# Performance work log

Measured on AMD Instinct MI355X. Metric: run time of the kernel, lower is better.

The kernel has to match this reference:

```python
import jax, jax.numpy as jnp
import numpy as np

B, NL, NT = 8, 64, 512   # graphs, ligand atoms/graph, target nodes/graph
CF = 128                 # per-node embedding dim (Linear(256,...) => 2*128)
H = 128                  # hidden_dim
K = 10                   # n_gaussians
E = 1024                 # ligand edges
BN_EPS = 1e-4


def setup_inputs() -> dict:
    key = jax.random.key(0)
    ks = jax.random.split(key, 24)
    inp = {}
    inp["h_l_x"] = jax.random.normal(ks[0], (B * NL, CF), jnp.float32)
    inp["h_t_x"] = jax.random.normal(ks[1], (B * NT, CF), jnp.float32)
    inp["h_l_pos"] = jax.random.normal(ks[2], (B * NL, 3), jnp.float32)
    inp["h_t_pos"] = jax.random.normal(ks[3], (B * NT, 3), jnp.float32)
    inp["edge_index"] = jax.random.randint(ks[4], (2, E), 0, B * NL, jnp.int64)
    s = 0.05
    inp["W1"] = jax.random.normal(ks[5], (2 * CF, H), jnp.float32) * s
    inp["b1"] = jnp.zeros((H,), jnp.float32)
    inp["gamma"] = jnp.ones((H,), jnp.float32)
    inp["beta"] = jnp.zeros((H,), jnp.float32)
    inp["rmean"] = jax.random.normal(ks[6], (H,), jnp.float32) * 0.1
    inp["rvar"] = jax.random.uniform(ks[7], (H,), jnp.float32, 0.5, 1.5)
    inp["Wpi"] = jax.random.normal(ks[8], (H, K), jnp.float32) * s
    inp["bpi"] = jnp.zeros((K,), jnp.float32)
    inp["Wsig"] = jax.random.normal(ks[9], (H, K), jnp.float32) * s
    inp["bsig"] = jnp.zeros((K,), jnp.float32)
    inp["Wmu"] = jax.random.normal(ks[10], (H, K), jnp.float32) * s
    inp["bmu"] = jnp.zeros((K,), jnp.float32)
    inp["Wat"] = jax.random.normal(ks[11], (CF, 28), jnp.float32) * s
    inp["bat"] = jnp.zeros((28,), jnp.float32)
    inp["Wbd"] = jax.random.normal(ks[12], (2 * CF, 6), jnp.float32) * s
    inp["bbd"] = jnp.zeros((6,), jnp.float32)
    return inp


def reference(h_l_x, h_t_x, h_l_pos, h_t_pos, edge_index,
              W1, b1, gamma, beta, rmean, rvar,
              Wpi, bpi, Wsig, bsig, Wmu, bmu, Wat, bat, Wbd, bbd):
    # dense batched node features (equal counts per graph => reshape)
    hl = h_l_x.reshape(B, NL, CF)
    ht = h_t_x.reshape(B, NT, CF)

    # cat([hl_repeat, ht_repeat]) @ W1 == hl@W1[:CF] + ht@W1[CF:] (broadcast add)
    zl = jnp.einsum('blc,ch->blh', hl, W1[:CF])          # [B,NL,H]
    zt = jnp.einsum('btc,ch->bth', ht, W1[CF:])          # [B,NT,H]
    z = zl[:, :, None, :] + zt[:, None, :, :] + b1       # [B,NL,NT,H]
    z = z.reshape(B * NL * NT, H)

    # BatchNorm1d (eval: running stats), ELU; Dropout is identity in eval
    z = (z - rmean) * (gamma / jnp.sqrt(rvar + BN_EPS)) + beta
    C = jax.nn.elu(z)

    pi = jax.nn.softmax(C @ Wpi + bpi, axis=-1)
    sigma = jax.nn.elu(C @ Wsig + bsig) + 1.1
    mu = jax.nn.elu(C @ Wmu + bmu) + 1.0

    # pairwise euclidean distances, detached in original
    pl = h_l_pos.reshape(B, NL, 3)
    pt = h_t_pos.reshape(B, NT, 3)
    d2 = (-2.0 * jnp.einsum('bld,btd->blt', pl, pt)
          + jnp.sum(pt ** 2, -1)[:, None, :]
          + jnp.sum(pl ** 2, -1)[:, :, None])
    dist = jnp.sqrt(d2).reshape(B * NL * NT)
    dist = jax.lax.stop_gradient(dist)[:, None]          # [P,1]

    atom_types = h_l_x @ Wat + bat                       # [B*NL,28]
    eb = jnp.concatenate([h_l_x[edge_index[0]], h_l_x[edge_index[1]]], axis=1)
    bond_types = eb @ Wbd + bbd                          # [E,6]

    C_batch = jnp.repeat(jnp.arange(B, dtype=jnp.int32), NL * NT)
    return (pi, sigma, mu, dist, atom_types, bond_types, C_batch)
```

## Files before the change

### kernel.cpp

```cpp
#include <hip/hip_runtime.h>
#include <cstdint>
#include <cstddef>

#define NB_B 8
#define NL   64
#define NT   512
#define CF   128
#define HD   128
#define NK   10
#define NE   1024

static constexpr size_t P_TOT    = (size_t)NB_B * NL * NT;
static constexpr size_t PI_OFF   = 0;
static constexpr size_t SIG_OFF  = P_TOT * 10;
static constexpr size_t MU_OFF   = SIG_OFF + P_TOT * 10;
static constexpr size_t DIST_OFF = MU_OFF + P_TOT * 10;
static constexpr size_t AT_OFF   = DIST_OFF + P_TOT;
static constexpr size_t BD_OFF   = AT_OFF + 512 * 28;
static constexpr size_t CB_OFF   = BD_OFF + NE * 6;

typedef __attribute__((ext_vector_type(8))) short short8;
typedef __attribute__((ext_vector_type(4))) float floatx4;
typedef __attribute__((ext_vector_type(2))) float floatx2;

__device__ __forceinline__ float bf2f(unsigned short u) {
    return __uint_as_float(((unsigned int)u) << 16);
}
__device__ __forceinline__ unsigned short f2bf(float f) {
    unsigned int x = __float_as_uint(f);
    x = (x + 0x7FFFu + ((x >> 16) & 1u)) >> 16;
    return (unsigned short)x;
}

__global__ __launch_bounds__(256) void k_pre(
    const float* __restrict__ hl,
    const float* __restrict__ ht,
    const int*   __restrict__ eidx,
    const float* __restrict__ W1,
    const float* __restrict__ b1,
    const float* __restrict__ gamma_,
    const float* __restrict__ beta_,
    const float* __restrict__ rmean,
    const float* __restrict__ rvar,
    const float* __restrict__ Wpi,
    const float* __restrict__ Wsig,
    const float* __restrict__ Wmu,
    const float* __restrict__ Wat,
    const float* __restrict__ bat,
    const float* __restrict__ Wbd,
    const float* __restrict__ bbd,
    unsigned short* __restrict__ zl,
    unsigned short* __restrict__ zt,
    unsigned short* __restrict__ wcomb,
    float* __restrict__ out_at,
    float* __restrict__ out_bd)
{
    const int blk = blockIdx.x;
    const int tid = threadIdx.x;

    if (blk < 576) {
        __shared__ float xs[8 * CF];
        const int r0 = blk * 8;
        const bool is_l = (r0 < 512);
        const float* src = is_l ? (hl + (size_t)r0 * CF)
                                : (ht + (size_t)(r0 - 512) * CF);
        for (int i = tid; i < 8 * CF; i += 256) xs[i] = src[i];
        __syncthreads();

        const int h  = tid & 127;
        const int rr = (tid >> 7) * 4;
        float a0 = 0.f, a1 = 0.f, a2 = 0.f, a3 = 0.f;
        const float* wp = W1 + (size_t)(is_l ? 0 : CF) * HD + h;
        #pragma unroll 4
        for (int c = 0; c < CF; ++c) {
            float w = wp[(size_t)c * HD];
            a0 += xs[(rr + 0) * CF + c] * w;
            a1 += xs[(rr + 1) * CF + c] * w;
            a2 += xs[(rr + 2) * CF + c] * w;
            a3 += xs[(rr + 3) * CF + c] * w;
        }
        const float s = gamma_[h] * rsqrtf(rvar[h] + 1e-4f);
        if (is_l) {
            zl[(size_t)(r0 + rr + 0) * HD + h] = f2bf(a0 * s);
            zl[(size_t)(r0 + rr + 1) * HD + h] = f2bf(a1 * s);
            zl[(size_t)(r0 + rr + 2) * HD + h] = f2bf(a2 * s);
            zl[(size_t)(r0 + rr + 3) * HD + h] = f2bf(a3 * s);
        } else {
            const float off = (b1[h] - rmean[h]) * s + beta_[h];
            const int rt = r0 - 512 + rr;
            zt[(size_t)(rt + 0) * HD + h] = f2bf(a0 * s + off);
            zt[(size_t)(rt + 1) * HD + h] = f2bf(a1 * s + off);
            zt[(size_t)(rt + 2) * HD + h] = f2bf(a2 * s + off);
            zt[(size_t)(rt + 3) * HD + h] = f2bf(a3 * s + off);
        }
    } else if (blk == 576) {
        for (int i = tid; i < HD * 32; i += 256) {
            int hh = i >> 5, n = i & 31;
            float v = 0.f;
            if (n < 10)      v = Wpi [hh * NK + n];
            else if (n < 20) v = Wsig[hh * NK + (n - 10)];
            else if (n < 30) v = Wmu [hh * NK + (n - 20)];
            wcomb[i] = f2bf(v);
        }
    } else if (blk < 633) {
        const int oi = (blk - 577) * 256 + tid;
        const int r = oi / 28, n = oi - r * 28;
        float acc = bat[n];
        #pragma unroll 4
        for (int c = 0; c < CF; ++c)
            acc += hl[(size_t)r * CF + c] * Wat[c * 28 + n];
        out_at[oi] = acc;
    } else {
        const int oi = (blk - 633) * 256 + tid;
        const int e = oi / 6, n = oi - e * 6;
        const int s0 = eidx[e], s1 = eidx[NE + e];
        float acc = bbd[n];
        #pragma unroll 4
        for (int c = 0; c < CF; ++c) {
            acc += hl[(size_t)s0 * CF + c] * Wbd[c * 6 + n];
            acc += hl[(size_t)s1 * CF + c] * Wbd[(CF + c) * 6 + n];
        }
        out_bd[oi] = acc;
    }
}

__global__ __launch_bounds__(256) void k_main(
    const unsigned short* __restrict__ zl,
    const unsigned short* __restrict__ zt,
    const unsigned short* __restrict__ wcomb,
    const float* __restrict__ bpi,
    const float* __restrict__ bsig,
    const float* __restrict__ bmu,
    const float* __restrict__ hlpos,
    const float* __restrict__ htpos,
    float* __restrict__ out)
{
    __shared__ unsigned short Cl[128 * 136];
    __shared__ float Dl[128 * 33];
    __shared__ float zls[HD];
    __shared__ float biass[32];
    __shared__ float pls[4];

    const int tid  = threadIdx.x;
    const int blk  = blockIdx.x;
    const int b    = blk >> 6;
    const int l    = blk & 63;
    const int lane = tid & 63;
    const int wave = tid >> 6;

    if (tid < 128) {
        zls[tid] = bf2f(zl[(size_t)(b * NL + l) * HD + tid]);
    } else if (tid < 160) {
        int n = tid - 128;
        float v = 0.f;
        if (n < 10)      v = bpi[n];
        else if (n < 20) v = bsig[n - 10];
        else if (n < 30) v = bmu[n - 20];
        biass[n] = v;
    } else if (tid < 163) {
        pls[tid - 160] = hlpos[(size_t)(b * NL + l) * 3 + (tid - 160)];
    }

    short8 bfrag[2][4];
    #pragma unroll
    for (int nt = 0; nt < 2; ++nt) {
        #pragma unroll
        for (int kb = 0; kb < 4; ++kb) {
            const int n = nt * 16 + (lane & 15);
            const int kbase = kb * 32 + (lane >> 4) * 8;
            #pragma unroll
            for (int j = 0; j < 8; ++j)
                bfrag[nt][kb][j] = (short)wcomb[(kbase + j) * 32 + n];
        }
    }
    __syncthreads();

    for (int ch = 0; ch < 4; ++ch) {
        const int tc = ch * 128;

        {
            const int p  = tid >> 1;
            const int h0 = (tid & 1) * 64;
            const unsigned short* ztr = zt + (size_t)(b * NT + tc + p) * HD + h0;
            #pragma unroll
            for (int hh = 0; hh < 64; hh += 8) {
                short8 zv = *(const short8*)(ztr + hh);
                short8 cv;
                #pragma unroll
                for (int e2 = 0; e2 < 8; ++e2) {
                    float a = zls[h0 + hh + e2] + bf2f((unsigned short)zv[e2]);
                    float c = (a > 0.f) ? a : (__expf(a) - 1.f);
                    cv[e2] = (short)f2bf(c);
                }
                *(short8*)(&Cl[p * 136 + h0 + hh]) = cv;
            }
        }
        __syncthreads();

        floatx4 acc[2][2];
        #pragma unroll
        for (int i = 0; i < 2; ++i)
            #pragma unroll
            for (int j = 0; j < 2; ++j)
                acc[i][j] = (floatx4){0.f, 0.f, 0.f, 0.f};

        const int m = lane & 15;
        #pragma unroll
        for (int kb = 0; kb < 4; ++kb) {
            const int ko = kb * 32 + (lane >> 4) * 8;
            short8 a0 = *(const short8*)(&Cl[(wave * 32 + m) * 136 + ko]);
            short8 a1 = *(const short8*)(&Cl[(wave * 32 + 16 + m) * 136 + ko]);
            #pragma unroll
            for (int nt = 0; nt < 2; ++nt) {
                acc[0][nt] = __builtin_amdgcn_mfma_f32_16x16x32_bf16(a0, bfrag[nt][kb], acc[0][nt], 0, 0, 0);
                acc[1][nt] = __builtin_amdgcn_mfma_f32_16x16x32_bf16(a1, bfrag[nt][kb], acc[1][nt], 0, 0, 0);
            }
        }
        #pragma unroll
        for (int pt = 0; pt < 2; ++pt)
            #pragma unroll
            for (int nt = 0; nt < 2; ++nt)
                #pragma unroll
                for (int r = 0; r < 4; ++r) {
                    const int row = wave * 32 + pt * 16 + (lane >> 4) * 4 + r;
                    const int col = nt * 16 + (lane & 15);
                    Dl[row * 33 + col] = acc[pt][nt][r];
                }
        __syncthreads();

        const size_t gp = ((size_t)(b * NL + l)) * NT + tc + (tid & 127);
        if (tid < 128) {
            const int p = tid;
            float v[10];
            float mx = -1e30f;
            #pragma unroll
            for (int n = 0; n < 10; ++n) {
                v[n] = Dl[p * 33 + n] + biass[n];
                mx = fmaxf(mx, v[n]);
            }
            float s = 0.f;
            #pragma unroll
            for (int n = 0; n < 10; ++n) { v[n] = __expf(v[n] - mx); s += v[n]; }
            const float inv = 1.f / s;
            floatx2* po = (floatx2*)(out + PI_OFF + gp * 10);
            #pragma unroll
            for (int n = 0; n < 5; ++n) po[n] = (floatx2){v[2*n] * inv, v[2*n+1] * inv};
        } else {
            const int p = tid - 128;
            float sg[10], mv[10];
            #pragma unroll
            for (int n = 0; n < 10; ++n) {
                float x = Dl[p * 33 + 10 + n] + biass[10 + n];
                sg[n] = ((x > 0.f) ? x : (__expf(x) - 1.f)) + 1.1f;
                float y = Dl[p * 33 + 20 + n] + biass[20 + n];
                mv[n] = ((y > 0.f) ? y : (__expf(y) - 1.f)) + 1.0f;
            }
            floatx2* ps = (floatx2*)(out + SIG_OFF + gp * 10);
            floatx2* pm = (floatx2*)(out + MU_OFF  + gp * 10);
            #pragma unroll
            for (int n = 0; n < 5; ++n) {
                ps[n] = (floatx2){sg[2*n], sg[2*n+1]};
                pm[n] = (floatx2){mv[2*n], mv[2*n+1]};
            }
            const int t = tc + p;
            const size_t pb = (size_t)(b * NT + t) * 3;
            const float dx = pls[0] - htpos[pb + 0];
            const float dy = pls[1] - htpos[pb + 1];
            const float dz = pls[2] - htpos[pb + 2];
            out[DIST_OFF + gp] = sqrtf(dx * dx + dy * dy + dz * dz);
            out[CB_OFF + gp]   = (float)b;
        }
        __syncthreads();
    }
}

extern "C" void kernel_launch(void* const* d_in, const int* in_sizes, int n_in,
                              void* d_out, int out_size, void* d_ws, size_t ws_size,
                              hipStream_t stream)
{
    const float* hl     = (const float*)d_in[0];
    const float* ht     = (const float*)d_in[1];
    const float* hlpos  = (const float*)d_in[2];
    const float* htpos  = (const float*)d_in[3];
    const int*   eidx   = (const int*)d_in[4];
    const float* W1     = (const float*)d_in[5];
    const float* b1     = (const float*)d_in[6];
    const float* gamma_ = (const float*)d_in[7];
    const float* beta_  = (const float*)d_in[8];
    const float* rmean  = (const float*)d_in[9];
    const float* rvar   = (const float*)d_in[10];
    const float* Wpi    = (const float*)d_in[11];
    const float* bpi    = (const float*)d_in[12];
    const float* Wsig   = (const float*)d_in[13];
    const float* bsig   = (const float*)d_in[14];
    const float* Wmu    = (const float*)d_in[15];
    const float* bmu    = (const float*)d_in[16];
    const float* Wat    = (const float*)d_in[17];
    const float* bat    = (const float*)d_in[18];
    const float* Wbd    = (const float*)d_in[19];
    const float* bbd    = (const float*)d_in[20];

    float* out = (float*)d_out;
    unsigned short* ws  = (unsigned short*)d_ws;
    unsigned short* zl    = ws;
    unsigned short* zt    = ws + 512 * 128;
    unsigned short* wcomb = ws + 512 * 128 + 4096 * 128;

    k_pre<<<657, 256, 0, stream>>>(hl, ht, eidx, W1, b1, gamma_, beta_, rmean, rvar,
                                   Wpi, Wsig, Wmu, Wat, bat, Wbd, bbd,
                                   zl, zt, wcomb, out + AT_OFF, out + BD_OFF);
    k_main<<<512, 256, 0, stream>>>(zl, zt, wcomb, bpi, bsig, bmu, hlpos, htpos, out);
}
```

Measured before the change: 139.6 us.

## Split main kernel per target chunk, build MFMA A-fragments in registers, MFMA pre-GEMM

k_main now launches one block per (graph, ligand atom, 128-target chunk) instead of looping over four chunks, so there are four times as many blocks and fewer serial iterations each. The ELU-activated C tile is built directly in registers from global zt and zl loads, skipping the LDS staging buffer and one barrier per chunk. The combined head weights are stored transposed so each B fragment is a single vector load. The zl/zt projection in k_pre moves from a scalar FP32 loop to bf16 MFMA with in-register conversion. The costs are redundant zl and bias loads across blocks and bf16 rounding of the inputs and W1 in the projection.

```diff
diff --git a/kernel.cpp b/kernel.cpp
--- a/kernel.cpp
+++ b/kernel.cpp
@@ -51,59 +51,87 @@
     const float* __restrict__ bbd,
     unsigned short* __restrict__ zl,
     unsigned short* __restrict__ zt,
-    unsigned short* __restrict__ wcomb,
+    unsigned short* __restrict__ wcomb_t,
     float* __restrict__ out_at,
     float* __restrict__ out_bd)
 {
     const int blk = blockIdx.x;
     const int tid = threadIdx.x;
 
-    if (blk < 576) {
-        __shared__ float xs[8 * CF];
-        const int r0 = blk * 8;
-        const bool is_l = (r0 < 512);
-        const float* src = is_l ? (hl + (size_t)r0 * CF)
-                                : (ht + (size_t)(r0 - 512) * CF);
-        for (int i = tid; i < 8 * CF; i += 256) xs[i] = src[i];
-        __syncthreads();
-
-        const int h  = tid & 127;
-        const int rr = (tid >> 7) * 4;
-        float a0 = 0.f, a1 = 0.f, a2 = 0.f, a3 = 0.f;
-        const float* wp = W1 + (size_t)(is_l ? 0 : CF) * HD + h;
-        #pragma unroll 4
-        for (int c = 0; c < CF; ++c) {
-            float w = wp[(size_t)c * HD];
-            a0 += xs[(rr + 0) * CF + c] * w;
-            a1 += xs[(rr + 1) * CF + c] * w;
-            a2 += xs[(rr + 2) * CF + c] * w;
-            a3 += xs[(rr + 3) * CF + c] * w;
-        }
-        const float s = gamma_[h] * rsqrtf(rvar[h] + 1e-4f);
-        if (is_l) {
-            zl[(size_t)(r0 + rr + 0) * HD + h] = f2bf(a0 * s);
-            zl[(size_t)(r0 + rr + 1) * HD + h] = f2bf(a1 * s);
-            zl[(size_t)(r0 + rr + 2) * HD + h] = f2bf(a2 * s);
-            zl[(size_t)(r0 + rr + 3) * HD + h] = f2bf(a3 * s);
-        } else {
-            const float off = (b1[h] - rmean[h]) * s + beta_[h];
-            const int rt = r0 - 512 + rr;
-            zt[(size_t)(rt + 0) * HD + h] = f2bf(a0 * s + off);
-            zt[(size_t)(rt + 1) * HD + h] = f2bf(a1 * s + off);
-            zt[(size_t)(rt + 2) * HD + h] = f2bf(a2 * s + off);
-            zt[(size_t)(rt + 3) * HD + h] = f2bf(a3 * s + off);
-        }
-    } else if (blk == 576) {
-        for (int i = tid; i < HD * 32; i += 256) {
-            int hh = i >> 5, n = i & 31;
+    if (blk < 144) {
+        const bool is_l = (blk < 16);
+        const int rbase = is_l ? blk * 32 : (blk - 16) * 32;
+        const float* A  = is_l ? hl : ht;
+        const float* Wx = W1 + (is_l ? 0 : (size_t)CF * HD);
+        unsigned short* Z = is_l ? zl : zt;
+
+        const int wave = tid >> 6;
+        const int lane = tid & 63;
+        const int m    = lane & 15;
+        const int kq   = (lane >> 4) * 8;
+        const int n0   = wave * 32 + m;
+
+        floatx4 acc[2][2];
+        #pragma unroll
+        for (int i = 0; i < 2; ++i)
+            #pragma unroll
+            for (int j = 0; j < 2; ++j)
+                acc[i][j] = (floatx4){0.f, 0.f, 0.f, 0.f};
+
+        #pragma unroll
+        for (int kb = 0; kb < 4; ++kb) {
+            const int k0 = kb * 32 + kq;
+            short8 a[2];
+            #pragma unroll
+            for (int mt = 0; mt < 2; ++mt) {
+                const float* ap = A + (size_t)(rbase + mt * 16 + m) * CF + k0;
+                floatx4 f0 = *(const floatx4*)ap;
+                floatx4 f1 = *(const floatx4*)(ap + 4);
+                #pragma unroll
+                for (int j = 0; j < 4; ++j) {
+                    a[mt][j]     = (short)f2bf(f0[j]);
+                    a[mt][4 + j] = (short)f2bf(f1[j]);
+                }
+            }
+            short8 bf[2];
+            #pragma unroll
+            for (int nt = 0; nt < 2; ++nt) {
+                const int n = n0 + nt * 16;
+                #pragma unroll
+                for (int j = 0; j < 8; ++j)
+                    bf[nt][j] = (short)f2bf(Wx[(size_t)(k0 + j) * HD + n]);
+            }
+            #pragma unroll
+            for (int mt = 0; mt < 2; ++mt)
+                #pragma unroll
+                for (int nt = 0; nt < 2; ++nt)
+                    acc[mt][nt] = __builtin_amdgcn_mfma_f32_16x16x32_bf16(a[mt], bf[nt], acc[mt][nt], 0, 0, 0);
+        }
+
+        #pragma unroll
+        for (int nt = 0; nt < 2; ++nt) {
+            const int col = n0 + nt * 16;
+            const float s   = gamma_[col] * rsqrtf(rvar[col] + 1e-4f);
+            const float off = is_l ? 0.f : ((b1[col] - rmean[col]) * s + beta_[col]);
+            #pragma unroll
+            for (int mt = 0; mt < 2; ++mt)
+                #pragma unroll
+                for (int r = 0; r < 4; ++r) {
+                    const int row = rbase + mt * 16 + (lane >> 4) * 4 + r;
+                    Z[(size_t)row * HD + col] = f2bf(acc[mt][nt][r] * s + off);
+                }
+        }
+    } else if (blk == 144) {
+        for (int i = tid; i < 32 * HD; i += 256) {
+            const int n = i >> 7, k = i & 127;
             float v = 0.f;
-            if (n < 10)      v = Wpi [hh * NK + n];
-            else if (n < 20) v = Wsig[hh * NK + (n - 10)];
-            else if (n < 30) v = Wmu [hh * NK + (n - 20)];
-            wcomb[i] = f2bf(v);
-        }
-    } else if (blk < 633) {
-        const int oi = (blk - 577) * 256 + tid;
+            if (n < 10)      v = Wpi [k * NK + n];
+            else if (n < 20) v = Wsig[k * NK + (n - 10)];
+            else if (n < 30) v = Wmu [k * NK + (n - 20)];
+            wcomb_t[i] = f2bf(v);
+        }
+    } else if (blk < 201) {
+        const int oi = (blk - 145) * 256 + tid;
         const int r = oi / 28, n = oi - r * 28;
         float acc = bat[n];
         #pragma unroll 4
@@ -111,7 +139,7 @@
             acc += hl[(size_t)r * CF + c] * Wat[c * 28 + n];
         out_at[oi] = acc;
     } else {
-        const int oi = (blk - 633) * 256 + tid;
+        const int oi = (blk - 201) * 256 + tid;
         const int e = oi / 6, n = oi - e * 6;
         const int s0 = eidx[e], s1 = eidx[NE + e];
         float acc = bbd[n];
@@ -127,7 +155,7 @@
 __global__ __launch_bounds__(256) void k_main(
     const unsigned short* __restrict__ zl,
     const unsigned short* __restrict__ zt,
-    const unsigned short* __restrict__ wcomb,
+    const unsigned short* __restrict__ wcomb_t,
     const float* __restrict__ bpi,
     const float* __restrict__ bsig,
     const float* __restrict__ bmu,
@@ -135,142 +163,127 @@
     const float* __restrict__ htpos,
     float* __restrict__ out)
 {
-    __shared__ unsigned short Cl[128 * 136];
     __shared__ float Dl[128 * 33];
-    __shared__ float zls[HD];
     __shared__ float biass[32];
-    __shared__ float pls[4];
+    __shared__ float pls[3];
 
     const int tid  = threadIdx.x;
     const int blk  = blockIdx.x;
-    const int b    = blk >> 6;
-    const int l    = blk & 63;
+    const int b    = blk >> 8;
+    const int l    = (blk >> 2) & 63;
+    const int ch   = blk & 3;
     const int lane = tid & 63;
     const int wave = tid >> 6;
-
-    if (tid < 128) {
-        zls[tid] = bf2f(zl[(size_t)(b * NL + l) * HD + tid]);
-    } else if (tid < 160) {
-        int n = tid - 128;
+    const int m    = lane & 15;
+    const int kq   = (lane >> 4) * 8;
+
+    if (tid < 32) {
         float v = 0.f;
-        if (n < 10)      v = bpi[n];
-        else if (n < 20) v = bsig[n - 10];
-        else if (n < 30) v = bmu[n - 20];
-        biass[n] = v;
-    } else if (tid < 163) {
-        pls[tid - 160] = hlpos[(size_t)(b * NL + l) * 3 + (tid - 160)];
+        if (tid < 10)      v = bpi[tid];
+        else if (tid < 20) v = bsig[tid - 10];
+        else if (tid < 30) v = bmu[tid - 20];
+        biass[tid] = v;
+    } else if (tid < 35) {
+        pls[tid - 32] = hlpos[(size_t)(b * NL + l) * 3 + (tid - 32)];
     }
 
     short8 bfrag[2][4];
     #pragma unroll
-    for (int nt = 0; nt < 2; ++nt) {
-        #pragma unroll
-        for (int kb = 0; kb < 4; ++kb) {
-            const int n = nt * 16 + (lane & 15);
-            const int kbase = kb * 32 + (lane >> 4) * 8;
-            #pragma unroll
-            for (int j = 0; j < 8; ++j)
-                bfrag[nt][kb][j] = (short)wcomb[(kbase + j) * 32 + n];
-        }
+    for (int nt = 0; nt < 2; ++nt)
+        #pragma unroll
+        for (int kb = 0; kb < 4; ++kb)
+            bfrag[nt][kb] = *(const short8*)(wcomb_t + (size_t)(nt * 16 + m) * HD + kb * 32 + kq);
+
+    const unsigned short* zlr = zl + (size_t)(b * NL + l) * HD;
+    const unsigned short* ztb = zt + (size_t)(b * NT + ch * 128) * HD;
+
+    floatx4 acc[2][2];
+    #pragma unroll
+    for (int i = 0; i < 2; ++i)
+        #pragma unroll
+        for (int j = 0; j < 2; ++j)
+            acc[i][j] = (floatx4){0.f, 0.f, 0.f, 0.f};
+
+    #pragma unroll
+    for (int kb = 0; kb < 4; ++kb) {
+        const int k0 = kb * 32 + kq;
+        short8 zlv = *(const short8*)(zlr + k0);
+        float zf[8];
+        #pragma unroll
+        for (int j = 0; j < 8; ++j) zf[j] = bf2f((unsigned short)zlv[j]);
+
+        short8 a[2];
+        #pragma unroll
+        for (int mt = 0; mt < 2; ++mt) {
+            const int row = wave * 32 + mt * 16 + m;
+            short8 ztv = *(const short8*)(ztb + (size_t)row * HD + k0);
+            #pragma unroll
+            for (int j = 0; j < 8; ++j) {
+                const float x = zf[j] + bf2f((unsigned short)ztv[j]);
+                const float c = (x > 0.f) ? x : (__expf(x) - 1.f);
+                a[mt][j] = (short)f2bf(c);
+            }
+        }
+        #pragma unroll
+        for (int mt = 0; mt < 2; ++mt)
+            #pragma unroll
+            for (int nt = 0; nt < 2; ++nt)
+                acc[mt][nt] = __builtin_amdgcn_mfma_f32_16x16x32_bf16(a[mt], bfrag[nt][kb], acc[mt][nt], 0, 0, 0);
     }
+
+    #pragma unroll
+    for (int mt = 0; mt < 2; ++mt)
+        #pragma unroll
+        for (int nt = 0; nt < 2; ++nt)
+            #pragma unroll
+            for (int r = 0; r < 4; ++r) {
+                const int row = wave * 32 + mt * 16 + (lane >> 4) * 4 + r;
+                const int col = nt * 16 + m;
+                Dl[row * 33 + col] = acc[mt][nt][r];
+            }
     __syncthreads();
 
-    for (int ch = 0; ch < 4; ++ch) {
-        const int tc = ch * 128;
-
-        {
-            const int p  = tid >> 1;
-            const int h0 = (tid & 1) * 64;
-            const unsigned short* ztr = zt + (size_t)(b * NT + tc + p) * HD + h0;
-            #pragma unroll
-            for (int hh = 0; hh < 64; hh += 8) {
-                short8 zv = *(const short8*)(ztr + hh);
-                short8 cv;
-                #pragma unroll
-                for (int e2 = 0; e2 < 8; ++e2) {
-                    float a = zls[h0 + hh + e2] + bf2f((unsigned short)zv[e2]);
-                    float c = (a > 0.f) ? a : (__expf(a) - 1.f);
-                    cv[e2] = (short)f2bf(c);
-                }
-                *(short8*)(&Cl[p * 136 + h0 + hh]) = cv;
-            }
-        }
-        __syncthreads();
-
-        floatx4 acc[2][2];
-        #pragma unroll
-        for (int i = 0; i < 2; ++i)
-            #pragma unroll
-            for (int j = 0; j < 2; ++j)
-                acc[i][j] = (floatx4){0.f, 0.f, 0.f, 0.f};
-
-        const int m = lane & 15;
-        #pragma unroll
-        for (int kb = 0; kb < 4; ++kb) {
-            const int ko = kb * 32 + (lane >> 4) * 8;
-            short8 a0 = *(const short8*)(&Cl[(wave * 32 + m) * 136 + ko]);
-            short8 a1 = *(const short8*)(&Cl[(wave * 32 + 16 + m) * 136 + ko]);
-            #pragma unroll
-            for (int nt = 0; nt < 2; ++nt) {
-                acc[0][nt] = __builtin_amdgcn_mfma_f32_16x16x32_bf16(a0, bfrag[nt][kb], acc[0][nt], 0, 0, 0);
-                acc[1][nt] = __builtin_amdgcn_mfma_f32_16x16x32_bf16(a1, bfrag[nt][kb], acc[1][nt], 0, 0, 0);
-            }
-        }
-        #pragma unroll
-        for (int pt = 0; pt < 2; ++pt)
-            #pragma unroll
-            for (int nt = 0; nt < 2; ++nt)
-                #pragma unroll
-                for (int r = 0; r < 4; ++r) {
-                    const int row = wave * 32 + pt * 16 + (lane >> 4) * 4 + r;
-                    const int col = nt * 16 + (lane & 15);
-                    Dl[row * 33 + col] = acc[pt][nt][r];
-                }
-        __syncthreads();
-
-        const size_t gp = ((size_t)(b * NL + l)) * NT + tc + (tid & 127);
-        if (tid < 128) {
-            const int p = tid;
-            float v[10];
-            float mx = -1e30f;
-            #pragma unroll
-            for (int n = 0; n < 10; ++n) {
-                v[n] = Dl[p * 33 + n] + biass[n];
-                mx = fmaxf(mx, v[n]);
-            }
-            float s = 0.f;
-            #pragma unroll
-            for (int n = 0; n < 10; ++n) { v[n] = __expf(v[n] - mx); s += v[n]; }
-            const float inv = 1.f / s;
-            floatx2* po = (floatx2*)(out + PI_OFF + gp * 10);
-            #pragma unroll
-            for (int n = 0; n < 5; ++n) po[n] = (floatx2){v[2*n] * inv, v[2*n+1] * inv};
-        } else {
-            const int p = tid - 128;
-            float sg[10], mv[10];
-            #pragma unroll
-            for (int n = 0; n < 10; ++n) {
-                float x = Dl[p * 33 + 10 + n] + biass[10 + n];
-                sg[n] = ((x > 0.f) ? x : (__expf(x) - 1.f)) + 1.1f;
-                float y = Dl[p * 33 + 20 + n] + biass[20 + n];
-                mv[n] = ((y > 0.f) ? y : (__expf(y) - 1.f)) + 1.0f;
-            }
-            floatx2* ps = (floatx2*)(out + SIG_OFF + gp * 10);
-            floatx2* pm = (floatx2*)(out + MU_OFF  + gp * 10);
-            #pragma unroll
-            for (int n = 0; n < 5; ++n) {
-                ps[n] = (floatx2){sg[2*n], sg[2*n+1]};
-                pm[n] = (floatx2){mv[2*n], mv[2*n+1]};
-            }
-            const int t = tc + p;
-            const size_t pb = (size_t)(b * NT + t) * 3;
-            const float dx = pls[0] - htpos[pb + 0];
-            const float dy = pls[1] - htpos[pb + 1];
-            const float dz = pls[2] - htpos[pb + 2];
-            out[DIST_OFF + gp] = sqrtf(dx * dx + dy * dy + dz * dz);
-            out[CB_OFF + gp]   = (float)b;
-        }
-        __syncthreads();
+    const size_t gp = ((size_t)(b * NL + l)) * NT + ch * 128 + (tid & 127);
+    if (tid < 128) {
+        const int p = tid;
+        float v[10];
+        float mx = -1e30f;
+        #pragma unroll
+        for (int n = 0; n < 10; ++n) {
+            v[n] = Dl[p * 33 + n] + biass[n];
+            mx = fmaxf(mx, v[n]);
+        }
+        float s = 0.f;
+        #pragma unroll
+        for (int n = 0; n < 10; ++n) { v[n] = __expf(v[n] - mx); s += v[n]; }
+        const float inv = 1.f / s;
+        floatx2* po = (floatx2*)(out + PI_OFF + gp * 10);
+        #pragma unroll
+        for (int n = 0; n < 5; ++n) po[n] = (floatx2){v[2*n] * inv, v[2*n+1] * inv};
+    } else {
+        const int p = tid - 128;
+        float sg[10], mv[10];
+        #pragma unroll
+        for (int n = 0; n < 10; ++n) {
+            const float x = Dl[p * 33 + 10 + n] + biass[10 + n];
+            sg[n] = ((x > 0.f) ? x : (__expf(x) - 1.f)) + 1.1f;
+            const float y = Dl[p * 33 + 20 + n] + biass[20 + n];
+            mv[n] = ((y > 0.f) ? y : (__expf(y) - 1.f)) + 1.0f;
+        }
+        floatx2* ps = (floatx2*)(out + SIG_OFF + gp * 10);
+        floatx2* pm = (floatx2*)(out + MU_OFF  + gp * 10);
+        #pragma unroll
+        for (int n = 0; n < 5; ++n) {
+            ps[n] = (floatx2){sg[2*n], sg[2*n+1]};
+            pm[n] = (floatx2){mv[2*n], mv[2*n+1]};
+        }
+        const int t = ch * 128 + p;
+        const size_t pb = (size_t)(b * NT + t) * 3;
+        const float dx = pls[0] - htpos[pb + 0];
+        const float dy = pls[1] - htpos[pb + 1];
+        const float dz = pls[2] - htpos[pb + 2];
+        out[DIST_OFF + gp] = sqrtf(dx * dx + dy * dy + dz * dz);
+        out[CB_OFF + gp]   = (float)b;
     }
 }
 
@@ -302,12 +315,12 @@
 
     float* out = (float*)d_out;
     unsigned short* ws  = (unsigned short*)d_ws;
-    unsigned short* zl    = ws;
-    unsigned short* zt    = ws + 512 * 128;
-    unsigned short* wcomb = ws + 512 * 128 + 4096 * 128;
-
-    k_pre<<<657, 256, 0, stream>>>(hl, ht, eidx, W1, b1, gamma_, beta_, rmean, rvar,
+    unsigned short* zl      = ws;
+    unsigned short* zt      = ws + 512 * 128;
+    unsigned short* wcomb_t = ws + 512 * 128 + 4096 * 128;
+
+    k_pre<<<225, 256, 0, stream>>>(hl, ht, eidx, W1, b1, gamma_, beta_, rmean, rvar,
                                    Wpi, Wsig, Wmu, Wat, bat, Wbd, bbd,
-                                   zl, zt, wcomb, out + AT_OFF, out + BD_OFF);
-    k_main<<<512, 256, 0, stream>>>(zl, zt, wcomb, bpi, bsig, bmu, hlpos, htpos, out);
-}
+                                   zl, zt, wcomb_t, out + AT_OFF, out + BD_OFF);
+    k_main<<<2048, 256, 0, stream>>>(zl, zt, wcomb_t, bpi, bsig, bmu, hlpos, htpos, out);
+}
```

After: 137.4 us. Within noise of the previous version (-1.6%).
